# Kernel tuning notes

Measured on AMD Instinct MI355X. Metric: run time of the kernel, lower is better.

Reference implementation:

```python
import jax, jax.numpy as jnp
import numpy as np

K_STEPS = 10
ALPHA = 0.9
N_NODES = 16384
N_CLASSES = 64
N_EDGES = 524288


def setup_inputs() -> dict:
    key = jax.random.key(0)
    k1, k2, k3 = jax.random.split(key, 3)
    masked_y_true = jax.random.normal(k1, (N_NODES, N_CLASSES), dtype=jnp.float32)
    K = jax.random.normal(k2, (N_NODES, N_NODES), dtype=jnp.float32)
    edge_index = jax.random.randint(k3, (2, N_EDGES), 0, N_NODES, dtype=jnp.int32)
    return {"masked_y_true": masked_y_true, "K": K, "edge_index": edge_index}


def reference(masked_y_true, K, edge_index):
    src, dst = edge_index[0], edge_index[1]
    # DAD normalization: w_e = deg(src)^-1/2 * deg(dst)^-1/2
    deg = jnp.zeros((N_NODES,), jnp.float32).at[dst].add(1.0)
    dinv = jax.lax.rsqrt(jnp.maximum(deg, 1.0))
    w = dinv[src] * dinv[dst]  # [E]

    def spmm(x):
        # A @ x with A in edge-list form (static sparsity, reused each step)
        return jax.ops.segment_sum(w[:, None] * x[src], dst, num_segments=N_NODES)

    def prop_step(_, y):
        return ALPHA * spmm(y) + (1.0 - ALPHA) * y

    y = jax.lax.fori_loop(0, K_STEPS, prop_step, masked_y_true)
    y = K @ y
    y = jax.lax.fori_loop(0, K_STEPS, prop_step, y)
    return y
```

## Files before the change

### kernel.cpp

```cpp
#include <hip/hip_runtime.h>

#define NN 16384
#define NC 64
#define NE 524288
#define ALPHA 0.9f
#define KSTEPS 10

typedef _Float16 f16;
typedef _Float16 f16x4 __attribute__((ext_vector_type(4)));
typedef _Float16 f16x8 __attribute__((ext_vector_type(8)));
typedef float f32x4 __attribute__((ext_vector_type(4)));
typedef int i32x16 __attribute__((ext_vector_type(16)));

__global__ __launch_bounds__(256) void deg_kernel(const int* __restrict__ dst,
                                                  unsigned* __restrict__ deg) {
    int e = blockIdx.x * 256 + threadIdx.x;
    atomicAdd(&deg[dst[e]], 1u);
}

__global__ __launch_bounds__(1024) void scan_kernel(const unsigned* __restrict__ deg,
                                                    float* __restrict__ dinv,
                                                    unsigned* __restrict__ rowoff,
                                                    unsigned* __restrict__ cursor) {
    __shared__ unsigned part[1024];
    const int t = threadIdx.x;
    const int base = t * 16;
    unsigned local[16];
    unsigned s = 0;
    #pragma unroll
    for (int i = 0; i < 16; ++i) {
        local[i] = s;
        s += (deg[base + i] + 7u) & ~7u;
    }
    part[t] = s;
    __syncthreads();
    for (int off = 1; off < 1024; off <<= 1) {
        unsigned v = (t >= off) ? part[t - off] : 0u;
        __syncthreads();
        part[t] += v;
        __syncthreads();
    }
    const unsigned ex = (t == 0) ? 0u : part[t - 1];
    #pragma unroll
    for (int i = 0; i < 16; ++i) {
        unsigned ro = ex + local[i];
        rowoff[base + i] = ro;
        cursor[base + i] = ro;
        unsigned d = deg[base + i];
        dinv[base + i] = rsqrtf(fmaxf((float)d, 1.0f));
    }
    if (t == 1023) rowoff[NN] = part[1023];
}

__global__ __launch_bounds__(256) void fill_kernel(const int* __restrict__ src,
                                                   const int* __restrict__ dst,
                                                   const float* __restrict__ dinv,
                                                   unsigned* __restrict__ cursor,
                                                   int2* __restrict__ csr) {
    int e = blockIdx.x * 256 + threadIdx.x;
    int s = src[e], d = dst[e];
    float w = dinv[s] * dinv[d];
    unsigned p = atomicAdd(&cursor[d], 1u);
    csr[p] = make_int2(s, __float_as_int(w));
}

__global__ __launch_bounds__(256) void prop_kernel(const float* __restrict__ x,
                                                   float* __restrict__ y,
                                                   const unsigned* __restrict__ rowoff,
                                                   const int* __restrict__ csr) {
    const int lane = threadIdx.x & 63;
    const int n = __builtin_amdgcn_readfirstlane(blockIdx.x * 4 + (threadIdx.x >> 6));
    const unsigned beg = rowoff[n];
    const unsigned nb = (rowoff[n + 1] - beg) >> 3;
    float acc0 = 0.f, acc1 = 0.f;
    if (nb) {
        i32x16 e = *(const i32x16*)(csr + 2 * beg);
        for (unsigned b = 1; b < nb; ++b) {
            float xv[8];
            #pragma unroll
            for (int j = 0; j < 8; ++j)
                xv[j] = x[(unsigned)e[2 * j] * 64u + lane];
            const i32x16 f = *(const i32x16*)(csr + 2 * (beg + b * 8));
            #pragma unroll
            for (int j = 0; j < 8; ++j) {
                const float w = __int_as_float(e[2 * j + 1]);
                if (j & 1) acc1 = fmaf(w, xv[j], acc1);
                else       acc0 = fmaf(w, xv[j], acc0);
            }
            e = f;
        }
        float xv[8];
        #pragma unroll
        for (int j = 0; j < 8; ++j)
            xv[j] = x[(unsigned)e[2 * j] * 64u + lane];
        #pragma unroll
        for (int j = 0; j < 8; ++j) {
            const float w = __int_as_float(e[2 * j + 1]);
            if (j & 1) acc1 = fmaf(w, xv[j], acc1);
            else       acc0 = fmaf(w, xv[j], acc0);
        }
    }
    y[n * 64 + lane] = ALPHA * (acc0 + acc1) + (1.0f - ALPHA) * x[n * 64 + lane];
}

__global__ __launch_bounds__(256) void ysplit_kernel(const float* __restrict__ y,
                                                     f16* __restrict__ yhT,
                                                     f16* __restrict__ ylT) {
    __shared__ f16 hb[64][72];
    __shared__ f16 lb[64][72];
    const int t = threadIdx.x;
    const int b = blockIdx.x;
    const int kl = t >> 2;
    const int cq = (t & 3) * 16;
    #pragma unroll
    for (int i = 0; i < 4; ++i) {
        float4 v = *(const float4*)&y[(size_t)(b * 64 + kl) * 64 + cq + i * 4];
        float vv[4] = {v.x, v.y, v.z, v.w};
        #pragma unroll
        for (int j = 0; j < 4; ++j) {
            int c = cq + i * 4 + j;
            f16 h = (f16)vv[j];
            float r = vv[j] - (float)h;
            hb[c][kl] = h;
            lb[c][kl] = (f16)r;
        }
    }
    __syncthreads();
    const int c = t >> 2;
    const int kq = (t & 3) * 16;
    #pragma unroll
    for (int s2 = 0; s2 < 2; ++s2) {
        int slot = (kq >> 3) + s2;
        int dslot = slot ^ (c & 7);
        f16x8 hv, lv;
        #pragma unroll
        for (int j = 0; j < 8; ++j) { hv[j] = hb[c][kq + s2 * 8 + j]; lv[j] = lb[c][kq + s2 * 8 + j]; }
        *(f16x8*)&yhT[(size_t)c * NN + b * 64 + dslot * 8] = hv;
        *(f16x8*)&ylT[(size_t)c * NN + b * 64 + dslot * 8] = lv;
    }
}

__device__ inline void gload16(const void* g, void* l) {
    __builtin_amdgcn_global_load_lds((const __attribute__((address_space(1))) void*)g,
                                     (__attribute__((address_space(3))) void*)l, 16, 0, 0);
}

#define AH_OFF 0
#define AL_OFF 16384
#define YH_OFF 32768
#define YL_OFF 40960

__global__ __launch_bounds__(256, 3) void gemm_kernel(const float* __restrict__ A,
                                                      const f16* __restrict__ yhT,
                                                      const f16* __restrict__ ylT,
                                                      float* __restrict__ z) {
    __shared__ char lds[49152];
    const int t = threadIdx.x;
    const int w = t >> 6;
    const int l = t & 63;
    const size_t row0 = (size_t)blockIdx.x * 128;
    const int kbase = blockIdx.y * 2048;

    f32x4 acc[2][4];
    #pragma unroll
    for (int m = 0; m < 2; ++m)
        #pragma unroll
        for (int n = 0; n < 4; ++n)
            acc[m][n] = (f32x4){0.f, 0.f, 0.f, 0.f};

    const int arow_l = w * 4 + (l >> 4);
    const int acol = (l & 15) * 4;
    const int ycr = l >> 3;
    const int yco = (l & 7) * 8;

    float4 areg[8];
    #pragma unroll
    for (int i = 0; i < 8; ++i)
        areg[i] = *(const float4*)&A[(row0 + i * 16 + arow_l) * 16384 + kbase + acol];

    for (int tile = 0; tile < 32; ++tile) {
        const int kt = kbase + tile * 64;
        __syncthreads();
        #pragma unroll
        for (int j = 0; j < 2; ++j) {
            const int i = 2 * w + j;
            gload16(yhT + (size_t)(i * 8 + ycr) * NN + kt + yco, lds + YH_OFF + i * 1024);
            gload16(ylT + (size_t)(i * 8 + ycr) * NN + kt + yco, lds + YL_OFF + i * 1024);
        }
        #pragma unroll
        for (int i = 0; i < 8; ++i) {
            const int r = i * 16 + arow_l;
            float v[4] = {areg[i].x, areg[i].y, areg[i].z, areg[i].w};
            f16x4 h4, l4;
            #pragma unroll
            for (int j = 0; j < 4; ++j) {
                f16 h = (f16)v[j];
                h4[j] = h;
                l4[j] = (f16)(v[j] - (float)h);
            }
            const int byte = r * 128 + (((((l & 15) >> 1)) ^ (r & 7)) << 4) + (l & 1) * 8;
            *(f16x4*)(lds + AH_OFF + byte) = h4;
            *(f16x4*)(lds + AL_OFF + byte) = l4;
        }
        __syncthreads();
        const int ktn = kbase + ((tile < 31) ? (tile + 1) : 31) * 64;
        #pragma unroll
        for (int i = 0; i < 8; ++i)
            areg[i] = *(const float4*)&A[(row0 + i * 16 + arow_l) * 16384 + ktn + acol];
        #pragma unroll
        for (int s = 0; s < 2; ++s) {
            const int slot = s * 4 + (l >> 4);
            f16x8 ah[2], alo[2];
            #pragma unroll
            for (int m = 0; m < 2; ++m) {
                const int r = w * 32 + m * 16 + (l & 15);
                const int byte = r * 128 + ((slot ^ (r & 7)) << 4);
                ah[m]  = *(const f16x8*)(lds + AH_OFF + byte);
                alo[m] = *(const f16x8*)(lds + AL_OFF + byte);
            }
            #pragma unroll
            for (int n = 0; n < 4; ++n) {
                const int c = n * 16 + (l & 15);
                const int byte = c * 128 + ((slot ^ (c & 7)) << 4);
                const f16x8 bh = *(const f16x8*)(lds + YH_OFF + byte);
                const f16x8 bl = *(const f16x8*)(lds + YL_OFF + byte);
                #pragma unroll
                for (int m = 0; m < 2; ++m) {
                    acc[m][n] = __builtin_amdgcn_mfma_f32_16x16x32_f16(ah[m],  bh, acc[m][n], 0, 0, 0);
                    acc[m][n] = __builtin_amdgcn_mfma_f32_16x16x32_f16(ah[m],  bl, acc[m][n], 0, 0, 0);
                    acc[m][n] = __builtin_amdgcn_mfma_f32_16x16x32_f16(alo[m], bh, acc[m][n], 0, 0, 0);
                }
            }
        }
    }
    #pragma unroll
    for (int m = 0; m < 2; ++m)
        #pragma unroll
        for (int n = 0; n < 4; ++n)
            #pragma unroll
            for (int q = 0; q < 4; ++q) {
                const size_t gr = row0 + w * 32 + m * 16 + (l >> 4) * 4 + q;
                const int gc = n * 16 + (l & 15);
                atomicAdd(&z[gr * 64 + gc], acc[m][n][q]);
            }
}

extern "C" void kernel_launch(void* const* d_in, const int* in_sizes, int n_in,
                              void* d_out, int out_size, void* d_ws, size_t ws_size,
                              hipStream_t stream) {
    const float* ytrue = (const float*)d_in[0];
    const float* Kmat  = (const float*)d_in[1];
    const int*   eidx  = (const int*)d_in[2];
    const int* esrc = eidx;
    const int* edst = eidx + NE;
    float* out = (float*)d_out;

    char* ws = (char*)d_ws;
    size_t off = 0;
    auto alloc = [&](size_t bytes) -> void* {
        void* p = ws + off;
        off += (bytes + 255) & ~(size_t)255;
        return p;
    };
    const size_t CSR_ENTRIES = (size_t)NE + 8 * NN;
    unsigned* deg    = (unsigned*)alloc((size_t)NN * 4);
    unsigned* rowoff = (unsigned*)alloc((size_t)(NN + 1) * 4);
    unsigned* cursor = (unsigned*)alloc((size_t)NN * 4);
    float*    dinv   = (float*)alloc((size_t)NN * 4);
    int2*     csr    = (int2*)alloc(CSR_ENTRIES * 8);
    float*    yA     = (float*)alloc((size_t)NN * NC * 4);
    float*    yB     = (float*)alloc((size_t)NN * NC * 4);
    f16*      yhT    = (f16*)alloc((size_t)NC * NN * 2);
    f16*      ylT    = (f16*)alloc((size_t)NC * NN * 2);

    hipMemsetAsync(deg, 0, (size_t)NN * 4, stream);
    hipMemsetAsync(csr, 0, CSR_ENTRIES * 8, stream);
    deg_kernel<<<NE / 256, 256, 0, stream>>>(edst, deg);
    scan_kernel<<<1, 1024, 0, stream>>>(deg, dinv, rowoff, cursor);
    fill_kernel<<<NE / 256, 256, 0, stream>>>(esrc, edst, dinv, cursor, csr);

    const float* cur = ytrue;
    float* bufs[2] = {yA, yB};
    int pb = 0;
    for (int s = 0; s < KSTEPS; ++s) {
        float* nxt = bufs[pb];
        pb ^= 1;
        prop_kernel<<<NN / 4, 256, 0, stream>>>(cur, nxt, rowoff, (const int*)csr);
        cur = nxt;
    }

    ysplit_kernel<<<NN / 64, 256, 0, stream>>>(cur, yhT, ylT);

    float* z = (cur == yA) ? yB : yA;
    hipMemsetAsync(z, 0, (size_t)NN * NC * 4, stream);
    gemm_kernel<<<dim3(128, 8), 256, 0, stream>>>(Kmat, yhT, ylT, z);

    float* other = (z == yA) ? yB : yA;
    const float* c2 = z;
    for (int s = 0; s < KSTEPS; ++s) {
        float* nxt = (s == KSTEPS - 1) ? out : other;
        prop_kernel<<<NN / 4, 256, 0, stream>>>(c2, nxt, rowoff, (const int*)csr);
        other = (float*)c2;
        c2 = nxt;
    }
}
```

Before: 543.0 us.

## Double-buffer GEMM Y tiles with explicit waitcnt pipeline and widen SpMM edge batches

The GEMM now double-buffers the Y tiles in LDS and keeps two register sets of A loads in flight. It uses explicit s_waitcnt and s_barrier scheduling so global loads overlap the MFMA work, and drops occupancy from 3 to 2 blocks per CU to make room for the 64KB LDS. The SpMM pads each CSR row to 16 edges and processes two 8-edge groups per iteration, so more gather loads are in flight. The cost is extra padding work on low-degree rows and lower GEMM occupancy.

```diff
diff --git a/kernel.cpp b/kernel.cpp
--- a/kernel.cpp
+++ b/kernel.cpp
@@ -11,6 +11,9 @@
 typedef _Float16 f16x8 __attribute__((ext_vector_type(8)));
 typedef float f32x4 __attribute__((ext_vector_type(4)));
 typedef int i32x16 __attribute__((ext_vector_type(16)));
+
+#define MEMB   asm volatile("" ::: "memory")
+#define SCHED0 __builtin_amdgcn_sched_barrier(0)
 
 __global__ __launch_bounds__(256) void deg_kernel(const int* __restrict__ dst,
                                                   unsigned* __restrict__ deg) {
@@ -30,7 +33,7 @@
     #pragma unroll
     for (int i = 0; i < 16; ++i) {
         local[i] = s;
-        s += (deg[base + i] + 7u) & ~7u;
+        s += (deg[base + i] + 15u) & ~15u;
     }
     part[t] = s;
     __syncthreads();
@@ -71,33 +74,48 @@
     const int lane = threadIdx.x & 63;
     const int n = __builtin_amdgcn_readfirstlane(blockIdx.x * 4 + (threadIdx.x >> 6));
     const unsigned beg = rowoff[n];
-    const unsigned nb = (rowoff[n + 1] - beg) >> 3;
+    const unsigned np = (rowoff[n + 1] - beg) >> 4;
     float acc0 = 0.f, acc1 = 0.f;
-    if (nb) {
-        i32x16 e = *(const i32x16*)(csr + 2 * beg);
-        for (unsigned b = 1; b < nb; ++b) {
-            float xv[8];
-            #pragma unroll
-            for (int j = 0; j < 8; ++j)
-                xv[j] = x[(unsigned)e[2 * j] * 64u + lane];
-            const i32x16 f = *(const i32x16*)(csr + 2 * (beg + b * 8));
+    if (np) {
+        i32x16 e0 = *(const i32x16*)(csr + 2 * beg);
+        i32x16 e1 = *(const i32x16*)(csr + 2 * beg + 16);
+        float xv0[8], xv1[8];
+        #pragma unroll
+        for (int j = 0; j < 8; ++j) xv0[j] = x[(unsigned)e0[2 * j] * 64u + lane];
+        #pragma unroll
+        for (int j = 0; j < 8; ++j) xv1[j] = x[(unsigned)e1[2 * j] * 64u + lane];
+        for (unsigned p = 1; p < np; ++p) {
+            const i32x16 f0 = *(const i32x16*)(csr + 2 * (beg + p * 16));
+            const i32x16 f1 = *(const i32x16*)(csr + 2 * (beg + p * 16) + 16);
             #pragma unroll
             for (int j = 0; j < 8; ++j) {
-                const float w = __int_as_float(e[2 * j + 1]);
-                if (j & 1) acc1 = fmaf(w, xv[j], acc1);
-                else       acc0 = fmaf(w, xv[j], acc0);
-            }
-            e = f;
-        }
-        float xv[8];
-        #pragma unroll
-        for (int j = 0; j < 8; ++j)
-            xv[j] = x[(unsigned)e[2 * j] * 64u + lane];
+                const float w = __int_as_float(e0[2 * j + 1]);
+                if (j & 1) acc1 = fmaf(w, xv0[j], acc1);
+                else       acc0 = fmaf(w, xv0[j], acc0);
+            }
+            #pragma unroll
+            for (int j = 0; j < 8; ++j) xv0[j] = x[(unsigned)f0[2 * j] * 64u + lane];
+            #pragma unroll
+            for (int j = 0; j < 8; ++j) {
+                const float w = __int_as_float(e1[2 * j + 1]);
+                if (j & 1) acc1 = fmaf(w, xv1[j], acc1);
+                else       acc0 = fmaf(w, xv1[j], acc0);
+            }
+            #pragma unroll
+            for (int j = 0; j < 8; ++j) xv1[j] = x[(unsigned)f1[2 * j] * 64u + lane];
+            e0 = f0; e1 = f1;
+        }
         #pragma unroll
         for (int j = 0; j < 8; ++j) {
-            const float w = __int_as_float(e[2 * j + 1]);
-            if (j & 1) acc1 = fmaf(w, xv[j], acc1);
-            else       acc0 = fmaf(w, xv[j], acc0);
+            const float w = __int_as_float(e0[2 * j + 1]);
+            if (j & 1) acc1 = fmaf(w, xv0[j], acc1);
+            else       acc0 = fmaf(w, xv0[j], acc0);
+        }
+        #pragma unroll
+        for (int j = 0; j < 8; ++j) {
+            const float w = __int_as_float(e1[2 * j + 1]);
+            if (j & 1) acc1 = fmaf(w, xv1[j], acc1);
+            else       acc0 = fmaf(w, xv1[j], acc0);
         }
     }
     y[n * 64 + lane] = ALPHA * (acc0 + acc1) + (1.0f - ALPHA) * x[n * 64 + lane];
@@ -147,14 +165,13 @@
 
 #define AH_OFF 0
 #define AL_OFF 16384
-#define YH_OFF 32768
-#define YL_OFF 40960
-
-__global__ __launch_bounds__(256, 3) void gemm_kernel(const float* __restrict__ A,
+#define YP_OFF 32768
+
+__global__ __launch_bounds__(256, 2) void gemm_kernel(const float* __restrict__ A,
                                                       const f16* __restrict__ yhT,
                                                       const f16* __restrict__ ylT,
                                                       float* __restrict__ z) {
-    __shared__ char lds[49152];
+    __shared__ char lds[65536];
     const int t = threadIdx.x;
     const int w = t >> 6;
     const int l = t & 63;
@@ -173,24 +190,30 @@
     const int ycr = l >> 3;
     const int yco = (l & 7) * 8;
 
-    float4 areg[8];
-    #pragma unroll
-    for (int i = 0; i < 8; ++i)
-        areg[i] = *(const float4*)&A[(row0 + i * 16 + arow_l) * 16384 + kbase + acol];
-
-    for (int tile = 0; tile < 32; ++tile) {
+    float4 aA[8], aB[8];
+
+    auto loadA = [&](float4 (&dst)[8], int tile) {
         const int kt = kbase + tile * 64;
-        __syncthreads();
+        #pragma unroll
+        for (int i = 0; i < 8; ++i)
+            dst[i] = *(const float4*)&A[(row0 + i * 16 + arow_l) * 16384 + kt + acol];
+    };
+    auto issueY = [&](int tile, int cur) {
+        const int kt = kbase + tile * 64;
         #pragma unroll
         for (int j = 0; j < 2; ++j) {
             const int i = 2 * w + j;
-            gload16(yhT + (size_t)(i * 8 + ycr) * NN + kt + yco, lds + YH_OFF + i * 1024);
-            gload16(ylT + (size_t)(i * 8 + ycr) * NN + kt + yco, lds + YL_OFF + i * 1024);
-        }
+            gload16(yhT + (size_t)(i * 8 + ycr) * NN + kt + yco,
+                    lds + YP_OFF + cur * 16384 + i * 1024);
+            gload16(ylT + (size_t)(i * 8 + ycr) * NN + kt + yco,
+                    lds + YP_OFF + cur * 16384 + 8192 + i * 1024);
+        }
+    };
+    auto writeA = [&](const float4 (&src)[8]) {
         #pragma unroll
         for (int i = 0; i < 8; ++i) {
             const int r = i * 16 + arow_l;
-            float v[4] = {areg[i].x, areg[i].y, areg[i].z, areg[i].w};
+            float v[4] = {src[i].x, src[i].y, src[i].z, src[i].w};
             f16x4 h4, l4;
             #pragma unroll
             for (int j = 0; j < 4; ++j) {
@@ -202,11 +225,8 @@
             *(f16x4*)(lds + AH_OFF + byte) = h4;
             *(f16x4*)(lds + AL_OFF + byte) = l4;
         }
-        __syncthreads();
-        const int ktn = kbase + ((tile < 31) ? (tile + 1) : 31) * 64;
-        #pragma unroll
-        for (int i = 0; i < 8; ++i)
-            areg[i] = *(const float4*)&A[(row0 + i * 16 + arow_l) * 16384 + ktn + acol];
+    };
+    auto mfmaTile = [&](int cur) {
         #pragma unroll
         for (int s = 0; s < 2; ++s) {
             const int slot = s * 4 + (l >> 4);
@@ -222,8 +242,8 @@
             for (int n = 0; n < 4; ++n) {
                 const int c = n * 16 + (l & 15);
                 const int byte = c * 128 + ((slot ^ (c & 7)) << 4);
-                const f16x8 bh = *(const f16x8*)(lds + YH_OFF + byte);
-                const f16x8 bl = *(const f16x8*)(lds + YL_OFF + byte);
+                const f16x8 bh = *(const f16x8*)(lds + YP_OFF + cur * 16384 + byte);
+                const f16x8 bl = *(const f16x8*)(lds + YP_OFF + cur * 16384 + 8192 + byte);
                 #pragma unroll
                 for (int m = 0; m < 2; ++m) {
                     acc[m][n] = __builtin_amdgcn_mfma_f32_16x16x32_f16(ah[m],  bh, acc[m][n], 0, 0, 0);
@@ -232,7 +252,43 @@
                 }
             }
         }
-    }
+    };
+
+    loadA(aA, 0); MEMB;
+    issueY(0, 0); MEMB;
+    loadA(aB, 1); MEMB;
+    writeA(aA);
+    asm volatile("s_waitcnt vmcnt(8)" ::: "memory");  SCHED0;
+    asm volatile("s_waitcnt lgkmcnt(0)" ::: "memory"); SCHED0;
+    __builtin_amdgcn_s_barrier(); SCHED0;
+
+#define GEMM_ITER(TILE, CUR, SETF, SETW)                                      \
+    issueY((TILE) + 1, (CUR) ^ 1); MEMB;                                      \
+    loadA(SETF, (TILE) + 2); MEMB;                                            \
+    mfmaTile(CUR);                                                            \
+    MEMB; SCHED0;                                                             \
+    __builtin_amdgcn_s_barrier();                 \
+    writeA(SETW);                                  \
+    asm volatile("s_waitcnt vmcnt(8)" ::: "memory");  SCHED0;   \
+    asm volatile("s_waitcnt lgkmcnt(0)" ::: "memory"); SCHED0;                \
+    __builtin_amdgcn_s_barrier(); SCHED0;
+
+    for (int tp = 0; tp < 15; ++tp) {
+        const int t0 = 2 * tp;
+        GEMM_ITER(t0,     0, aA, aB);
+        GEMM_ITER(t0 + 1, 1, aB, aA);
+    }
+    issueY(31, 1); MEMB;
+    mfmaTile(0);
+    MEMB; SCHED0;
+    __builtin_amdgcn_s_barrier();
+    writeA(aB);
+    asm volatile("s_waitcnt vmcnt(0)" ::: "memory");  SCHED0;
+    asm volatile("s_waitcnt lgkmcnt(0)" ::: "memory"); SCHED0;
+    __builtin_amdgcn_s_barrier(); SCHED0;
+    mfmaTile(1);
+#undef GEMM_ITER
+
     #pragma unroll
     for (int m = 0; m < 2; ++m)
         #pragma unroll
@@ -262,7 +318,7 @@
         off += (bytes + 255) & ~(size_t)255;
         return p;
     };
-    const size_t CSR_ENTRIES = (size_t)NE + 8 * NN;
+    const size_t CSR_ENTRIES = (size_t)NE + 16 * NN;
     unsigned* deg    = (unsigned*)alloc((size_t)NN * 4);
     unsigned* rowoff = (unsigned*)alloc((size_t)(NN + 1) * 4);
     unsigned* cursor = (unsigned*)alloc((size_t)NN * 4);
```

New measurement: 529.6 us. 1.03x faster.
